# Kernel optimization log

Hardware: AMD Instinct MI355X
Metric: run time of the kernel (lower is better)

The kernel has to match this reference:

```python
import jax, jax.numpy as jnp
import numpy as np

B, T, D = 4, 2048, 768
H = 12
DH = D // H
DFF = 3072
EPS = 1e-5


def _layernorm(x, g, b):
    mu = jnp.mean(x, axis=-1, keepdims=True)
    var = jnp.var(x, axis=-1, keepdims=True)
    return (x - mu) * jax.lax.rsqrt(var + EPS) * g + b


def setup_inputs() -> dict:
    key = jax.random.key(0)
    ks = jax.random.split(key, 12)
    s = lambda fan_in: 1.0 / np.sqrt(fan_in)
    return {
        "x": jax.random.normal(ks[0], (B, T, D), dtype=jnp.float32),
        "ln1_g": jnp.ones((D,), jnp.float32),
        "ln1_b": jnp.zeros((D,), jnp.float32),
        "w_qkv": jax.random.uniform(ks[1], (D, 3 * D), jnp.float32, -s(D), s(D)),
        "b_qkv": jax.random.uniform(ks[2], (3 * D,), jnp.float32, -s(D), s(D)),
        "w_proj": jax.random.uniform(ks[3], (D, D), jnp.float32, -s(D), s(D)),
        "b_proj": jax.random.uniform(ks[4], (D,), jnp.float32, -s(D), s(D)),
        "ln2_g": jnp.ones((D,), jnp.float32),
        "ln2_b": jnp.zeros((D,), jnp.float32),
        "w_ff1": jax.random.uniform(ks[5], (D, DFF), jnp.float32, -s(D), s(D)),
        "b_ff1": jax.random.uniform(ks[6], (DFF,), jnp.float32, -s(D), s(D)),
        "w_ff2": jax.random.uniform(ks[7], (DFF, D), jnp.float32, -s(DFF), s(DFF)),
        "b_ff2": jax.random.uniform(ks[8], (D,), jnp.float32, -s(DFF), s(DFF)),
    }


def reference(x, ln1_g, ln1_b, w_qkv, b_qkv, w_proj, b_proj,
              ln2_g, ln2_b, w_ff1, b_ff1, w_ff2, b_ff2):
    # --- attention sublayer ---
    h = _layernorm(x, ln1_g, ln1_b)
    qkv = h @ w_qkv + b_qkv                       # [B,T,3D]
    q, k, v = jnp.split(qkv, 3, axis=-1)
    q = q.reshape(B, T, H, DH).transpose(0, 2, 1, 3)  # [B,H,T,DH]
    k = k.reshape(B, T, H, DH).transpose(0, 2, 1, 3)
    v = v.reshape(B, T, H, DH).transpose(0, 2, 1, 3)
    att = jnp.einsum('bhqd,bhkd->bhqk', q, k) / jnp.sqrt(jnp.float32(DH))
    causal = jnp.tril(jnp.ones((T, T), dtype=bool))
    att = jnp.where(causal, att, -jnp.inf)
    att = jax.nn.softmax(att, axis=-1)
    out = jnp.einsum('bhqk,bhkd->bhqd', att, v)    # [B,H,T,DH]
    out = out.transpose(0, 2, 1, 3).reshape(B, T, D)
    x = x + out @ w_proj + b_proj
    # --- MLP sublayer ---
    h2 = _layernorm(x, ln2_g, ln2_b)
    h2 = jax.nn.gelu(h2 @ w_ff1 + b_ff1, approximate=False)
    x = x + h2 @ w_ff2 + b_ff2
    return x
```

## Files before the change

### kernel.cpp

```cpp
#include <hip/hip_runtime.h>
#include <cstdint>
#include <cstddef>

typedef unsigned short u16;
typedef unsigned int u32;
typedef __attribute__((ext_vector_type(8))) short s16x8;
typedef __attribute__((ext_vector_type(4))) float f32x4;

#define NB 4
#define NT 2048
#define ND 768
#define NH 12
#define NDH 64
#define NFF 3072
#define NM (NB*NT)

__device__ __forceinline__ u16 f2b(float f){
  union { float f; unsigned u; } c; c.f = f;
  unsigned r = c.u + 0x7fffu + ((c.u >> 16) & 1u);
  return (u16)(r >> 16);
}

__device__ __forceinline__ f32x4 mfma16(s16x8 a, s16x8 b, f32x4 c){
  return __builtin_amdgcn_mfma_f32_16x16x32_bf16(a, b, c, 0, 0, 0);
}

__device__ __forceinline__ void stage16(u16* lds, const u16* g){
  __builtin_amdgcn_global_load_lds(
      (const __attribute__((address_space(1))) unsigned int*)g,
      (__attribute__((address_space(3))) unsigned int*)lds,
      16, 0, 0);
}

__device__ __forceinline__ float gelu_f(float v){
  const float x = v * 0.70710678118654752f;
  const float ax = fabsf(x);
  const float t = 1.f / (1.f + 0.3275911f * ax);
  const float y = t * (0.254829592f + t * (-0.284496736f + t * (1.421413741f
                + t * (-1.453152027f + t * 1.061405429f))));
  float er = 1.f - y * __expf(-ax * ax);
  er = copysignf(er, x);
  return 0.5f * v * (1.f + er);
}

__global__ __launch_bounds__(256) void transpose_all(
    const float* __restrict__ w_qkv, const float* __restrict__ w_proj,
    const float* __restrict__ w_ff1, const float* __restrict__ w_ff2,
    u16* __restrict__ o_qkv, u16* __restrict__ o_proj,
    u16* __restrict__ o_ff1, u16* __restrict__ o_ff2)
{
  int bid = blockIdx.x;
  const float* in; u16* out; int K, N, nx;
  if (bid < 1728)      { in = w_qkv;  out = o_qkv;  K = 768;  N = 2304; nx = 72; }
  else if ((bid -= 1728) < 576)  { in = w_proj; out = o_proj; K = 768;  N = 768;  nx = 24; }
  else if ((bid -= 576) < 2304)  { in = w_ff1;  out = o_ff1;  K = 768;  N = 3072; nx = 96; }
  else { bid -= 2304;              in = w_ff2;  out = o_ff2;  K = 3072; N = 768;  nx = 24; }
  const int n0 = (bid % nx) * 32, k0 = (bid / nx) * 32;

  __shared__ float tile[32][33];
  const int tx = threadIdx.x, ty = threadIdx.y;
  #pragma unroll
  for (int i = 0; i < 32; i += 8)
    tile[ty + i][tx] = in[(size_t)(k0 + ty + i) * N + n0 + tx];
  __syncthreads();
  #pragma unroll
  for (int i = 0; i < 32; i += 8)
    out[(size_t)(n0 + ty + i) * K + k0 + tx] = f2b(tile[tx][ty + i]);
}

__global__ __launch_bounds__(256) void ln_kernel(
    const float* __restrict__ x, const float* __restrict__ g,
    const float* __restrict__ b, u16* __restrict__ out)
{
  const int row = blockIdx.x;
  const int t = threadIdx.x;
  const float* xr = x + (size_t)row * ND;
  float v0 = xr[t], v1 = xr[t + 256], v2 = xr[t + 512];
  float s = v0 + v1 + v2;
  float ss = v0*v0 + v1*v1 + v2*v2;
  #pragma unroll
  for (int o = 32; o; o >>= 1) { s += __shfl_xor(s, o, 64); ss += __shfl_xor(ss, o, 64); }
  __shared__ float red[8];
  const int w = t >> 6;
  if ((t & 63) == 0) { red[w] = s; red[4 + w] = ss; }
  __syncthreads();
  s  = red[0] + red[1] + red[2] + red[3];
  ss = red[4] + red[5] + red[6] + red[7];
  const float mu = s * (1.f / ND);
  const float var = ss * (1.f / ND) - mu * mu;
  const float rinv = rsqrtf(var + 1e-5f);
  u16* orow = out + (size_t)row * ND;
  orow[t]       = f2b((v0 - mu) * rinv * g[t]       + b[t]);
  orow[t + 256] = f2b((v1 - mu) * rinv * g[t + 256] + b[t + 256]);
  orow[t + 512] = f2b((v2 - mu) * rinv * g[t + 512] + b[t + 512]);
}

template<int EPI, int BM>
__global__ __launch_bounds__(256, (BM == 128) ? 3 : 4) void gemm_bt(
    const u16* __restrict__ A, const u16* __restrict__ Bt,
    const float* __restrict__ bias, const float* __restrict__ res,
    void* __restrict__ o0, void* __restrict__ o1, void* __restrict__ o2,
    const int M, const int N, const int K)
{
  constexpr int MI = BM / 64;
  __shared__ u16 As[3][BM * 32];
  __shared__ u16 Bs[3][128 * 32];
  const int tid = threadIdx.x;
  const int lane = tid & 63, wid = tid >> 6;
  const int wr = wid >> 1, wc = wid & 1;
  const int lg = lane >> 4, lm = lane & 15;
  const int bm = blockIdx.x * BM, bn = blockIdx.y * 128;

  f32x4 acc[2 * MI][4] = {};

  const int srow = tid >> 2;
  const int schunk = (tid & 3) ^ ((tid >> 3) & 3);
  const u16* ApT = A  + (size_t)(bm + srow) * K + schunk * 8;
  const u16* BpT = Bt + (size_t)(bn + srow) * K + schunk * 8;
  const size_t rs64 = (size_t)64 * K;
  const int woff = wid * 512;
  const int fswz = (lm >> 1) & 3;

  const int nt = K >> 5;

  #pragma unroll
  for (int p = 0; p < 2; ++p) {
    const int k0 = p << 5;
    stage16(&As[p][woff], ApT + k0);
    if (BM == 128) stage16(&As[p][woff + 2048], ApT + rs64 + k0);
    stage16(&Bs[p][woff],        BpT + k0);
    stage16(&Bs[p][woff + 2048], BpT + rs64 + k0);
  }

  for (int t = 0; t < nt; ++t) {
    if (t < nt - 1) {
      if (BM == 128) asm volatile("s_waitcnt vmcnt(4)" ::: "memory");
      else           asm volatile("s_waitcnt vmcnt(3)" ::: "memory");
    } else {
      asm volatile("s_waitcnt vmcnt(0)" ::: "memory");
    }
    __builtin_amdgcn_s_barrier();
    __builtin_amdgcn_sched_barrier(0);
    if (t + 2 < nt) {
      const int k0 = (t + 2) << 5;
      const int wb = (t + 2) % 3;
      stage16(&As[wb][woff], ApT + k0);
      if (BM == 128) stage16(&As[wb][woff + 2048], ApT + rs64 + k0);
      stage16(&Bs[wb][woff],        BpT + k0);
      stage16(&Bs[wb][woff + 2048], BpT + rs64 + k0);
    }
    __builtin_amdgcn_sched_barrier(0);
    const int rb = t % 3;
    s16x8 af[2 * MI], bf[4];
    #pragma unroll
    for (int i = 0; i < 2 * MI; i++)
      af[i] = *(const s16x8*)&As[rb][(wr * (BM / 2) + i * 16 + lm) * 32 + ((lg ^ fswz) * 8)];
    #pragma unroll
    for (int j = 0; j < 4; j++)
      bf[j] = *(const s16x8*)&Bs[rb][(wc * 64 + j * 16 + lm) * 32 + ((lg ^ fswz) * 8)];
    #pragma unroll
    for (int i = 0; i < 2 * MI; i++)
      #pragma unroll
      for (int j = 0; j < 4; j++)
        acc[i][j] = mfma16(af[i], bf[j], acc[i][j]);
  }

  #pragma unroll
  for (int i = 0; i < 2 * MI; i++)
    #pragma unroll
    for (int j = 0; j < 4; j++) {
      const int col = bn + wc * 64 + j * 16 + lm;
      const float bb = bias[col];
      #pragma unroll
      for (int r = 0; r < 4; r++) {
        const int row = bm + wr * (BM / 2) + i * 16 + lg * 4 + r;
        float v = acc[i][j][r] + bb;
        if (EPI == 0) {
          u16* dst; int rem;
          if (col < ND)            { dst = (u16*)o0; rem = col; v *= 0.125f; }
          else if (col < 2 * ND)   { dst = (u16*)o1; rem = col - ND; }
          else                     { dst = (u16*)o2; rem = col - 2 * ND; }
          const int hh = rem >> 6, dh = rem & 63;
          const int bb2 = row >> 11, tt = row & 2047;
          dst[(((size_t)bb2 * NH + hh) * NT + tt) * NDH + dh] = f2b(v);
        } else if (EPI == 1) {
          ((float*)o0)[(size_t)row * ND + col] = v + res[(size_t)row * ND + col];
        } else if (EPI == 2) {
          ((u16*)o0)[(size_t)row * NFF + col] = f2b(gelu_f(v));
        } else {
          ((float*)o0)[(size_t)row * ND + col] = v + res[(size_t)row * ND + col];
        }
      }
    }
}

__global__ __launch_bounds__(256,2) void attn_kernel(
    const u16* __restrict__ Q, const u16* __restrict__ Kg,
    const u16* __restrict__ V, u16* __restrict__ O)
{
  const int p  = blockIdx.y;
  const int bh = blockIdx.x;
  const int b = bh / NH, h = bh % NH;
  const int tid = threadIdx.x;
  const int lane = tid & 63, w = tid >> 6;
  const int lg = lane >> 4, lm = lane & 15;
  const int sr = tid >> 3;
  const int sc = (tid & 7) * 8;

  __shared__ u16 Ks[64 * 64];
  __shared__ u16 Vt[64 * 64];
  __shared__ u16 Ps[4][16 * 64];

  const u16* Qb = Q  + (size_t)bh * NT * NDH;
  const u16* Kb = Kg + (size_t)bh * NT * NDH;
  const u16* Vb = V  + (size_t)bh * NT * NDH;

  const int si0 = p, si1 = 31 - p;
  const int q00 = si0 * 64, q01 = si1 * 64;
  const int ktmax = si1;

  const s16x8 q0a = *(const s16x8*)&Qb[(size_t)(q00 + w * 16 + lm) * NDH + lg * 8];
  const s16x8 q0b = *(const s16x8*)&Qb[(size_t)(q00 + w * 16 + lm) * NDH + 32 + lg * 8];
  const s16x8 q1a = *(const s16x8*)&Qb[(size_t)(q01 + w * 16 + lm) * NDH + lg * 8];
  const s16x8 q1b = *(const s16x8*)&Qb[(size_t)(q01 + w * 16 + lm) * NDH + 32 + lg * 8];

  f32x4 oacc0[4] = {}, oacc1[4] = {};
  float m0 = -INFINITY, l0 = 0.f, m1 = -INFINITY, l1 = 0.f;

  auto do_strip = [&](const s16x8& qa, const s16x8& qb, f32x4* oacc,
                      float& m, float& l, bool diag) {
    f32x4 sv[4];
    #pragma unroll
    for (int n = 0; n < 4; ++n) {
      const int krow = (n * 16 + lm) * 64;
      const int swz = (lm & 7) << 3;
      s16x8 kf0 = *(const s16x8*)&Ks[krow + ((lg * 8) ^ swz)];
      s16x8 kf1 = *(const s16x8*)&Ks[krow + ((32 + lg * 8) ^ swz)];
      f32x4 s4 = {};
      s4 = mfma16(kf0, qa, s4);
      s4 = mfma16(kf1, qb, s4);
      sv[n] = s4;
    }
    if (diag) {
      #pragma unroll
      for (int n = 0; n < 4; ++n)
        #pragma unroll
        for (int r = 0; r < 4; ++r)
          if (n * 16 + lg * 4 + r > w * 16 + lm) sv[n][r] = -INFINITY;
    }
    float mx = -INFINITY;
    #pragma unroll
    for (int n = 0; n < 4; ++n)
      #pragma unroll
      for (int r = 0; r < 4; ++r) mx = fmaxf(mx, sv[n][r]);
    mx = fmaxf(mx, __shfl_xor(mx, 16));
    mx = fmaxf(mx, __shfl_xor(mx, 32));
    const float mnew = fmaxf(m, mx);
    const float alpha = __expf(m - mnew);
    m = mnew;

    float rs = 0.f;
    u32 pk[4][2];
    #pragma unroll
    for (int n = 0; n < 4; ++n) {
      const float p0 = __expf(sv[n][0] - mnew);
      const float p1 = __expf(sv[n][1] - mnew);
      const float p2 = __expf(sv[n][2] - mnew);
      const float p3 = __expf(sv[n][3] - mnew);
      rs += (p0 + p1) + (p2 + p3);
      pk[n][0] = (u32)f2b(p0) | ((u32)f2b(p1) << 16);
      pk[n][1] = (u32)f2b(p2) | ((u32)f2b(p3) << 16);
    }
    rs += __shfl_xor(rs, 16);
    rs += __shfl_xor(rs, 32);
    l = l * alpha + rs;

    #pragma unroll
    for (int n = 0; n < 4; ++n) {
      const int idx0 = lm * 64 + ((n * 16 + lg * 4) ^ ((lm & 7) << 3));
      *(u32*)&Ps[w][idx0] = pk[n][0];
      *(u32*)&Ps[w][idx0 + 2] = pk[n][1];
    }

    float av[4];
    #pragma unroll
    for (int r = 0; r < 4; ++r) av[r] = __shfl(alpha, lg * 4 + r);
    #pragma unroll
    for (int d = 0; d < 4; ++d)
      #pragma unroll
      for (int r = 0; r < 4; ++r) oacc[d][r] *= av[r];

    #pragma unroll
    for (int kh = 0; kh < 2; ++kh) {
      const s16x8 pf = *(const s16x8*)&Ps[w][lm * 64 + ((kh * 32 + lg * 8) ^ ((lm & 7) << 3))];
      #pragma unroll
      for (int dt = 0; dt < 4; ++dt) {
        const int g = ((2 * dt + (lm >> 3)) ^ (lm & 7)) & 7;
        const s16x8 vf = *(const s16x8*)&Vt[(dt * 16 + lm) * 64 + (((kh * 4 + lg) ^ g) << 3)];
        oacc[dt] = mfma16(pf, vf, oacc[dt]);
      }
    }
  };

  s16x8 kva = *(const s16x8*)&Kb[(size_t)sr * NDH + sc];
  s16x8 kvb = *(const s16x8*)&Kb[(size_t)(sr + 32) * NDH + sc];
  s16x8 vva = *(const s16x8*)&Vb[(size_t)sr * NDH + sc];
  s16x8 vvb = *(const s16x8*)&Vb[(size_t)(sr + 32) * NDH + sc];

  for (int kt = 0; kt <= ktmax; ++kt) {
    __syncthreads();
    *(s16x8*)&Ks[sr * 64 + (sc ^ ((sr & 7) << 3))] = kva;
    *(s16x8*)&Ks[(sr + 32) * 64 + (sc ^ ((sr & 7) << 3))] = kvb;
    #pragma unroll
    for (int e = 0; e < 8; ++e)
      Vt[(sc + e) * 64 + (sr ^ ((((tid & 7) ^ e)) << 3))] = (u16)vva[e];
    #pragma unroll
    for (int e = 0; e < 8; ++e)
      Vt[(sc + e) * 64 + ((sr + 32) ^ ((((tid & 7) ^ e)) << 3))] = (u16)vvb[e];
    __syncthreads();

    if (kt < ktmax) {
      const u16* Kn = Kb + (size_t)(kt + 1) * 64 * NDH;
      const u16* Vn = Vb + (size_t)(kt + 1) * 64 * NDH;
      kva = *(const s16x8*)&Kn[(size_t)sr * NDH + sc];
      kvb = *(const s16x8*)&Kn[(size_t)(sr + 32) * NDH + sc];
      vva = *(const s16x8*)&Vn[(size_t)sr * NDH + sc];
      vvb = *(const s16x8*)&Vn[(size_t)(sr + 32) * NDH + sc];
    }

    do_strip(q1a, q1b, oacc1, m1, l1, kt == si1);
    if (kt <= si0) do_strip(q0a, q0b, oacc0, m0, l0, kt == si0);
  }

  {
    float lv[4];
    #pragma unroll
    for (int r = 0; r < 4; ++r) lv[r] = 1.f / __shfl(l0, lg * 4 + r);
    #pragma unroll
    for (int dt = 0; dt < 4; ++dt)
      #pragma unroll
      for (int r = 0; r < 4; ++r) {
        const int qg = q00 + w * 16 + lg * 4 + r;
        O[((size_t)b * NT + qg) * ND + h * NDH + dt * 16 + lm] = f2b(oacc0[dt][r] * lv[r]);
      }
  }
  {
    float lv[4];
    #pragma unroll
    for (int r = 0; r < 4; ++r) lv[r] = 1.f / __shfl(l1, lg * 4 + r);
    #pragma unroll
    for (int dt = 0; dt < 4; ++dt)
      #pragma unroll
      for (int r = 0; r < 4; ++r) {
        const int qg = q01 + w * 16 + lg * 4 + r;
        O[((size_t)b * NT + qg) * ND + h * NDH + dt * 16 + lm] = f2b(oacc1[dt][r] * lv[r]);
      }
  }
}

extern "C" void kernel_launch(void* const* d_in, const int* in_sizes, int n_in,
                              void* d_out, int out_size, void* d_ws, size_t ws_size,
                              hipStream_t stream)
{
  const float* x      = (const float*)d_in[0];
  const float* ln1_g  = (const float*)d_in[1];
  const float* ln1_b  = (const float*)d_in[2];
  const float* w_qkv  = (const float*)d_in[3];
  const float* b_qkv  = (const float*)d_in[4];
  const float* w_proj = (const float*)d_in[5];
  const float* b_proj = (const float*)d_in[6];
  const float* ln2_g  = (const float*)d_in[7];
  const float* ln2_b  = (const float*)d_in[8];
  const float* w_ff1  = (const float*)d_in[9];
  const float* b_ff1  = (const float*)d_in[10];
  const float* w_ff2  = (const float*)d_in[11];
  const float* b_ff2  = (const float*)d_in[12];

  char* ws = (char*)d_ws;
  u16*   wt_qkv = (u16*)(ws + 0);
  u16*   wt_proj= (u16*)(ws + 3538944);
  u16*   wt_ff1 = (u16*)(ws + 4718592);
  u16*   wt_ff2 = (u16*)(ws + 9437184);
  u16*   hbuf   = (u16*)(ws + 14155776);
  u16*   qbuf   = (u16*)(ws + 26738688);
  u16*   kbuf   = (u16*)(ws + 39321600);
  u16*   vbuf   = (u16*)(ws + 51904512);
  u16*   aobuf  = (u16*)(ws + 64487424);
  float* x1     = (float*)(ws + 77070336);
  u16*   h2buf  = (u16*)(ws + 102236160);
  u16*   ff1buf = hbuf;

  transpose_all<<<6912, dim3(32,8), 0, stream>>>(w_qkv, w_proj, w_ff1, w_ff2,
                                                 wt_qkv, wt_proj, wt_ff1, wt_ff2);

  ln_kernel<<<NM, 256, 0, stream>>>(x, ln1_g, ln1_b, hbuf);
  gemm_bt<0,128><<<dim3(NM/128, 2304/128), 256, 0, stream>>>(hbuf, wt_qkv, b_qkv, nullptr,
                                                             qbuf, kbuf, vbuf, NM, 2304, ND);
  attn_kernel<<<dim3(NB*NH, 16), 256, 0, stream>>>(qbuf, kbuf, vbuf, aobuf);
  gemm_bt<1,64><<<dim3(NM/64, ND/128), 256, 0, stream>>>(aobuf, wt_proj, b_proj, x,
                                                         x1, nullptr, nullptr, NM, ND, ND);
  ln_kernel<<<NM, 256, 0, stream>>>(x1, ln2_g, ln2_b, h2buf);
  gemm_bt<2,128><<<dim3(NM/128, NFF/128), 256, 0, stream>>>(h2buf, wt_ff1, b_ff1, nullptr,
                                                            ff1buf, nullptr, nullptr, NM, NFF, ND);
  gemm_bt<3,64><<<dim3(NM/64, ND/128), 256, 0, stream>>>(ff1buf, wt_ff2, b_ff2, x1,
                                                         d_out, nullptr, nullptr, NM, ND, NFF);
}
```

Measured before the change: 281.8 us.

## Fuse weight transpose with first layernorm and defer attention rescaling

Merges the weight transpose/convert kernel and the first layernorm into one launch by appending layernorm blocks after the transpose blocks. In attention, the online-softmax rescale of the accumulator and running sum is skipped when the new tile max exceeds the running max by at most 8 across the whole wave, which saves exps and multiplies. The attention launch bound is raised to 3 blocks per CU to encourage higher occupancy, with a risk of register spills. The deferred max allows exponentials up to about e^8, which fits in fp32 and bf16 range but costs some precision.

```diff
diff --git a/kernel.cpp b/kernel.cpp
--- a/kernel.cpp
+++ b/kernel.cpp
@@ -43,12 +43,38 @@
   return 0.5f * v * (1.f + er);
 }
 
-__global__ __launch_bounds__(256) void transpose_all(
+__global__ __launch_bounds__(256) void pre_kernel(
     const float* __restrict__ w_qkv, const float* __restrict__ w_proj,
     const float* __restrict__ w_ff1, const float* __restrict__ w_ff2,
     u16* __restrict__ o_qkv, u16* __restrict__ o_proj,
-    u16* __restrict__ o_ff1, u16* __restrict__ o_ff2)
+    u16* __restrict__ o_ff1, u16* __restrict__ o_ff2,
+    const float* __restrict__ x, const float* __restrict__ ln_g,
+    const float* __restrict__ ln_b, u16* __restrict__ ln_out)
 {
+  const int t = threadIdx.x;
+  if (blockIdx.x >= 6912) {
+    const int row = blockIdx.x - 6912;
+    const float* xr = x + (size_t)row * ND;
+    float v0 = xr[t], v1 = xr[t + 256], v2 = xr[t + 512];
+    float s = v0 + v1 + v2;
+    float ss = v0*v0 + v1*v1 + v2*v2;
+    #pragma unroll
+    for (int o = 32; o; o >>= 1) { s += __shfl_xor(s, o, 64); ss += __shfl_xor(ss, o, 64); }
+    __shared__ float red[8];
+    const int w = t >> 6;
+    if ((t & 63) == 0) { red[w] = s; red[4 + w] = ss; }
+    __syncthreads();
+    s  = red[0] + red[1] + red[2] + red[3];
+    ss = red[4] + red[5] + red[6] + red[7];
+    const float mu = s * (1.f / ND);
+    const float var = ss * (1.f / ND) - mu * mu;
+    const float rinv = rsqrtf(var + 1e-5f);
+    u16* orow = ln_out + (size_t)row * ND;
+    orow[t]       = f2b((v0 - mu) * rinv * ln_g[t]       + ln_b[t]);
+    orow[t + 256] = f2b((v1 - mu) * rinv * ln_g[t + 256] + ln_b[t + 256]);
+    orow[t + 512] = f2b((v2 - mu) * rinv * ln_g[t + 512] + ln_b[t + 512]);
+    return;
+  }
   int bid = blockIdx.x;
   const float* in; u16* out; int K, N, nx;
   if (bid < 1728)      { in = w_qkv;  out = o_qkv;  K = 768;  N = 2304; nx = 72; }
@@ -58,7 +84,7 @@
   const int n0 = (bid % nx) * 32, k0 = (bid / nx) * 32;
 
   __shared__ float tile[32][33];
-  const int tx = threadIdx.x, ty = threadIdx.y;
+  const int tx = t & 31, ty = t >> 5;
   #pragma unroll
   for (int i = 0; i < 32; i += 8)
     tile[ty + i][tx] = in[(size_t)(k0 + ty + i) * N + n0 + tx];
@@ -194,7 +220,7 @@
     }
 }
 
-__global__ __launch_bounds__(256,2) void attn_kernel(
+__global__ __launch_bounds__(256,3) void attn_kernel(
     const u16* __restrict__ Q, const u16* __restrict__ Kg,
     const u16* __restrict__ V, u16* __restrict__ O)
 {
@@ -255,25 +281,29 @@
       for (int r = 0; r < 4; ++r) mx = fmaxf(mx, sv[n][r]);
     mx = fmaxf(mx, __shfl_xor(mx, 16));
     mx = fmaxf(mx, __shfl_xor(mx, 32));
-    const float mnew = fmaxf(m, mx);
-    const float alpha = __expf(m - mnew);
-    m = mnew;
+
+    const bool defer = __all(mx - m <= 8.f);
+    float alpha = 1.f;
+    if (!defer) {
+      const float mnew = fmaxf(m, mx);
+      alpha = __expf(m - mnew);
+      m = mnew;
+    }
 
     float rs = 0.f;
     u32 pk[4][2];
     #pragma unroll
     for (int n = 0; n < 4; ++n) {
-      const float p0 = __expf(sv[n][0] - mnew);
-      const float p1 = __expf(sv[n][1] - mnew);
-      const float p2 = __expf(sv[n][2] - mnew);
-      const float p3 = __expf(sv[n][3] - mnew);
+      const float p0 = __expf(sv[n][0] - m);
+      const float p1 = __expf(sv[n][1] - m);
+      const float p2 = __expf(sv[n][2] - m);
+      const float p3 = __expf(sv[n][3] - m);
       rs += (p0 + p1) + (p2 + p3);
       pk[n][0] = (u32)f2b(p0) | ((u32)f2b(p1) << 16);
       pk[n][1] = (u32)f2b(p2) | ((u32)f2b(p3) << 16);
     }
     rs += __shfl_xor(rs, 16);
     rs += __shfl_xor(rs, 32);
-    l = l * alpha + rs;
 
     #pragma unroll
     for (int n = 0; n < 4; ++n) {
@@ -282,13 +312,18 @@
       *(u32*)&Ps[w][idx0 + 2] = pk[n][1];
     }
 
-    float av[4];
-    #pragma unroll
-    for (int r = 0; r < 4; ++r) av[r] = __shfl(alpha, lg * 4 + r);
-    #pragma unroll
-    for (int d = 0; d < 4; ++d)
-      #pragma unroll
-      for (int r = 0; r < 4; ++r) oacc[d][r] *= av[r];
+    if (!defer) {
+      l = l * alpha + rs;
+      float av[4];
+      #pragma unroll
+      for (int r = 0; r < 4; ++r) av[r] = __shfl(alpha, lg * 4 + r);
+      #pragma unroll
+      for (int d = 0; d < 4; ++d)
+        #pragma unroll
+        for (int r = 0; r < 4; ++r) oacc[d][r] *= av[r];
+    } else {
+      l += rs;
+    }
 
     #pragma unroll
     for (int kh = 0; kh < 2; ++kh) {
@@ -390,10 +425,9 @@
   u16*   h2buf  = (u16*)(ws + 102236160);
   u16*   ff1buf = hbuf;
 
-  transpose_all<<<6912, dim3(32,8), 0, stream>>>(w_qkv, w_proj, w_ff1, w_ff2,
-                                                 wt_qkv, wt_proj, wt_ff1, wt_ff2);
-
-  ln_kernel<<<NM, 256, 0, stream>>>(x, ln1_g, ln1_b, hbuf);
+  pre_kernel<<<6912 + NM, 256, 0, stream>>>(w_qkv, w_proj, w_ff1, w_ff2,
+                                            wt_qkv, wt_proj, wt_ff1, wt_ff2,
+                                            x, ln1_g, ln1_b, hbuf);
   gemm_bt<0,128><<<dim3(NM/128, 2304/128), 256, 0, stream>>>(hbuf, wt_qkv, b_qkv, nullptr,
                                                              qbuf, kbuf, vbuf, NM, 2304, ND);
   attn_kernel<<<dim3(NB*NH, 16), 256, 0, stream>>>(qbuf, kbuf, vbuf, aobuf);
```

New measurement: 287.2 us. No clear change (+1.9%).
